# Performance work log

Hardware: AMD Instinct MI355X
Metric: run time of the kernel (lower is better)

Reference implementation:

```python
import jax, jax.numpy as jnp
import numpy as np

B, T, D, H = 4, 2048, 1024, 16
HD = D // H


def setup_inputs() -> dict:
    key = jax.random.key(0)
    kq, kk, kv, k1, k2, k3, k4 = jax.random.split(key, 7)
    q = jax.random.normal(kq, (B, T, D), dtype=jnp.float32)
    k = jax.random.normal(kk, (B, T, D), dtype=jnp.float32)
    v = jax.random.normal(kv, (B, T, D), dtype=jnp.float32)
    # causal mask, broadcast over heads: [B, 1, T, T]
    mask = jnp.broadcast_to(jnp.tril(jnp.ones((T, T), dtype=bool)), (B, 1, T, T))
    s = 0.02
    Wq = jax.random.normal(k1, (D, D), dtype=jnp.float32) * s
    Wk = jax.random.normal(k2, (D, D), dtype=jnp.float32) * s
    Wv = jax.random.normal(k3, (D, D), dtype=jnp.float32) * s
    Wo = jax.random.normal(k4, (D, D), dtype=jnp.float32) * s
    return {"q": q, "k": k, "v": v, "mask": mask,
            "Wq": Wq, "Wk": Wk, "Wv": Wv, "Wo": Wo}


def reference(q, k, v, mask, Wq, Wk, Wv, Wo):
    scale = HD ** -0.5
    # nn.Linear: y = x @ W.T  (bias=False)
    qh = (q @ Wq.T).reshape(B, T, H, HD).transpose(0, 2, 1, 3)  # [B,H,T,HD]
    kh = (k @ Wk.T).reshape(B, -1, H, HD).transpose(0, 2, 1, 3)
    vh = (v @ Wv.T).reshape(B, -1, H, HD).transpose(0, 2, 1, 3)
    scores = jnp.einsum('bhqd,bhkd->bhqk', qh, kh) * scale  # [B,H,T,T]
    # dropout p=0.0 -> identity (applied pre-mask in original)
    scores = jnp.where(mask, scores, -jnp.inf)
    probs = jax.nn.softmax(scores, axis=-1)
    attn = jnp.einsum('bhqk,bhkd->bhqd', probs, vh)  # [B,H,T,HD]
    attn = attn.transpose(0, 2, 1, 3).reshape(B, T, D)
    return attn @ Wo.T
```

## Files before the change

kernel.cpp:

```cpp
#include <hip/hip_runtime.h>
#include <stdint.h>

#define B_  4
#define T_  2048
#define D_  1024
#define H_  16
#define HD_ 64
#define KK_ 1024

typedef __bf16 bf16_t;
typedef __bf16 bf16x8 __attribute__((ext_vector_type(8)));
typedef float  f32x4  __attribute__((ext_vector_type(4)));
typedef float  f32x16 __attribute__((ext_vector_type(16)));

__device__ __forceinline__ uint16_t f2bf(float f) {
  uint32_t x = __float_as_uint(f);
  uint32_t r = (x + 0x7fffu + ((x >> 16) & 1u)) >> 16;
  return (uint16_t)r;
}

__device__ __forceinline__ uint32_t pack2(float a, float b) {
  return (uint32_t)f2bf(a) | ((uint32_t)f2bf(b) << 16);
}

__device__ __forceinline__ float exp2a(float x) {
  float r;
  asm("v_exp_f32 %0, %1" : "=v"(r) : "v"(x));
  return r;
}

__device__ __forceinline__ uint32_t cvtpk(float a, float b) {
  uint32_t r;
  asm("v_cvt_pk_bf16_f32 %0, %1, %2" : "=v"(r) : "v"(a), "v"(b));
  return r;
}

__device__ __forceinline__ void plswap(uint32_t& a, uint32_t& b) {
  asm("v_permlane32_swap_b32 %0, %1" : "+v"(a), "+v"(b));
}

__device__ __forceinline__ void gll16(const void* g, void* l) {
  __builtin_amdgcn_global_load_lds(
      (const __attribute__((address_space(1))) void*)g,
      (__attribute__((address_space(3))) void*)l, 16, 0, 0);
}

__global__ __launch_bounds__(256) void cvt3(const float* __restrict__ s0,
                                            const float* __restrict__ s1,
                                            const float* __restrict__ s2,
                                            uint16_t* __restrict__ d0,
                                            uint16_t* __restrict__ d1,
                                            uint16_t* __restrict__ d2) {
  const float* in = blockIdx.y == 0 ? s0 : (blockIdx.y == 1 ? s1 : s2);
  uint16_t* out = blockIdx.y == 0 ? d0 : (blockIdx.y == 1 ? d1 : d2);
  int i = (blockIdx.x * 256 + threadIdx.x) * 8;
  float4 a = *(const float4*)(in + i);
  float4 b = *(const float4*)(in + i + 4);
  uint4 u;
  u.x = pack2(a.x, a.y);
  u.y = pack2(a.z, a.w);
  u.z = pack2(b.x, b.y);
  u.w = pack2(b.z, b.w);
  *(uint4*)(out + i) = u;
}

__global__ __launch_bounds__(256) void cvtW(const float* __restrict__ s0,
                                            const float* __restrict__ s1,
                                            const float* __restrict__ s2,
                                            const float* __restrict__ s3,
                                            uint16_t* __restrict__ d0,
                                            uint16_t* __restrict__ d1,
                                            uint16_t* __restrict__ d2,
                                            uint16_t* __restrict__ d3) {
  const float* in = blockIdx.y == 0 ? s0 : (blockIdx.y == 1 ? s1 :
                    (blockIdx.y == 2 ? s2 : s3));
  uint16_t* out = blockIdx.y == 0 ? d0 : (blockIdx.y == 1 ? d1 :
                  (blockIdx.y == 2 ? d2 : d3));
  int i = (blockIdx.x * 256 + threadIdx.x) * 8;
  float4 a = *(const float4*)(in + i);
  float4 b = *(const float4*)(in + i + 4);
  uint4 u;
  u.x = pack2(a.x, a.y);
  u.y = pack2(a.z, a.w);
  u.z = pack2(b.x, b.y);
  u.w = pack2(b.z, b.w);
  *(uint4*)(out + i) = u;
}

__global__ __launch_bounds__(512, 2)
void gemm8(const uint16_t* __restrict__ a0, const uint16_t* __restrict__ a1,
           const uint16_t* __restrict__ a2, const uint16_t* __restrict__ w0,
           const uint16_t* __restrict__ w1, const uint16_t* __restrict__ w2,
           void* __restrict__ o0, void* __restrict__ o1, void* __restrict__ o2,
           int mode_base, float scale0) {
  __shared__ __align__(16) uint16_t Ab[3][128 * 64];
  __shared__ __align__(16) uint16_t Bb[3][256 * 64];

  const int nwg = gridDim.x;
  const int bid = blockIdx.x;
  const int cpx = nwg >> 3;
  const int swz = (bid & 7) * cpx + (bid >> 3);
  const int g = swz >> 8;
  const int r = swz & 255;
  const int mt = r >> 2, nt = r & 3;
  const int m0 = mt * 128, n0 = nt * 256;

  const uint16_t* A = g == 0 ? a0 : (g == 1 ? a1 : a2);
  const uint16_t* W = g == 0 ? w0 : (g == 1 ? w1 : w2);
  void* Out = g == 0 ? o0 : (g == 1 ? o1 : o2);
  const int mode = mode_base + g;
  const float scale = (mode == 0) ? scale0 : 1.0f;

  const int tid = threadIdx.x;
  const int wid = tid >> 6, lane = tid & 63;
  const int fr = lane & 15, fq = lane >> 4;
  const int wm = wid >> 2, wn = wid & 3;
  const int srow = lane >> 3, c8 = lane & 7;

  f32x4 acc[4][4];
#pragma unroll
  for (int i = 0; i < 4; ++i)
#pragma unroll
    for (int j = 0; j < 4; ++j) acc[i][j] = (f32x4){0.f, 0.f, 0.f, 0.f};

  const int NT = KK_ / 64;

#define STAGE(bi, t)                                                          \
  do {                                                                        \
    _Pragma("unroll")                                                         \
    for (int c = 0; c < 2; ++c) {                                             \
      int row = c * 64 + wid * 8 + srow;                                      \
      int sw = (c8 ^ (row & 7)) << 3;                                         \
      gll16(A + (size_t)(m0 + row) * KK_ + (t) * 64 + sw,                     \
            &Ab[bi][c * 4096 + wid * 512]);                                   \
    }                                                                         \
    _Pragma("unroll")                                                         \
    for (int c = 0; c < 4; ++c) {                                             \
      int row = c * 64 + wid * 8 + srow;                                      \
      int sw = (c8 ^ (row & 7)) << 3;                                         \
      gll16(W + (size_t)(n0 + row) * KK_ + (t) * 64 + sw,                     \
            &Bb[bi][c * 4096 + wid * 512]);                                   \
    }                                                                         \
  } while (0)

  STAGE(0, 0);
  STAGE(1, 1);
  asm volatile("s_waitcnt vmcnt(6)" ::: "memory");
  __builtin_amdgcn_s_barrier();

  int cur = 0;
  for (int t = 0; t < NT; ++t) {
    const uint16_t* Ac = &Ab[cur][0];
    const uint16_t* Bc = &Bb[cur][0];
    bf16x8 af0[4], bf0[4];
#pragma unroll
    for (int i = 0; i < 4; ++i) {
      int ra = wm * 64 + i * 16 + fr;
      af0[i] = *(const bf16x8*)&Ac[ra * 64 + ((fq ^ (ra & 7)) << 3)];
      int rb = wn * 64 + i * 16 + fr;
      bf0[i] = *(const bf16x8*)&Bc[rb * 64 + ((fq ^ (rb & 7)) << 3)];
    }
    if (t + 2 < NT) {
      int nb = cur + 2; if (nb >= 3) nb -= 3;
      STAGE(nb, t + 2);
    }
    bf16x8 af1[4], bf1[4];
#pragma unroll
    for (int i = 0; i < 4; ++i) {
      int ra = wm * 64 + i * 16 + fr;
      af1[i] = *(const bf16x8*)&Ac[ra * 64 + (((4 + fq) ^ (ra & 7)) << 3)];
      int rb = wn * 64 + i * 16 + fr;
      bf1[i] = *(const bf16x8*)&Bc[rb * 64 + (((4 + fq) ^ (rb & 7)) << 3)];
    }
    __builtin_amdgcn_s_setprio(1);
#pragma unroll
    for (int mf = 0; mf < 4; ++mf)
#pragma unroll
      for (int nf = 0; nf < 4; ++nf)
        acc[mf][nf] = __builtin_amdgcn_mfma_f32_16x16x32_bf16(af0[mf], bf0[nf],
                                                              acc[mf][nf], 0, 0, 0);
#pragma unroll
    for (int mf = 0; mf < 4; ++mf)
#pragma unroll
      for (int nf = 0; nf < 4; ++nf)
        acc[mf][nf] = __builtin_amdgcn_mfma_f32_16x16x32_bf16(af1[mf], bf1[nf],
                                                              acc[mf][nf], 0, 0, 0);
    __builtin_amdgcn_s_setprio(0);
    if (t + 1 < NT) {
      if (t + 2 < NT) {
        asm volatile("s_waitcnt vmcnt(6)" ::: "memory");
      } else {
        asm volatile("s_waitcnt vmcnt(0)" ::: "memory");
      }
      __builtin_amdgcn_s_barrier();
    }
    ++cur; if (cur == 3) cur = 0;
  }
#undef STAGE

#pragma unroll
  for (int mf = 0; mf < 4; ++mf) {
#pragma unroll
    for (int nf = 0; nf < 4; ++nf) {
      int m = m0 + wm * 64 + mf * 16 + fq * 4;
      int n = n0 + wn * 64 + nf * 16 + fr;
      if (mode == 2) {
        int b = m >> 11, t = m & (T_ - 1);
        int h = n >> 6, hd = n & 63;
        uint2 pk;
        pk.x = pack2(acc[mf][nf][0], acc[mf][nf][1]);
        pk.y = pack2(acc[mf][nf][2], acc[mf][nf][3]);
        uint16_t* dst = (uint16_t*)Out + ((((size_t)b * H_ + h) * HD_ + hd) * T_ + t);
        *(uint2*)dst = pk;
      } else if (mode == 3) {
#pragma unroll
        for (int rr = 0; rr < 4; ++rr)
          ((float*)Out)[(size_t)(m + rr) * D_ + n] = acc[mf][nf][rr];
      } else {
#pragma unroll
        for (int rr = 0; rr < 4; ++rr) {
          int mm = m + rr;
          int b = mm >> 11, t = mm & (T_ - 1);
          int h = n >> 6, hd = n & 63;
          ((uint16_t*)Out)[((((size_t)b * H_ + h) * T_ + t) << 6) + hd] =
              f2bf(acc[mf][nf][rr] * scale);
        }
      }
    }
  }
}

__global__ __launch_bounds__(512)
void attn_fwd(const uint16_t* __restrict__ Qh, const uint16_t* __restrict__ Kh,
              const uint16_t* __restrict__ Vt, uint16_t* __restrict__ O) {
  __shared__ __align__(16) uint16_t SB[6][64 * 64];

  const int tid = threadIdx.x, wid = tid >> 6, lane = tid & 63;
  const int ql = lane & 31, hi = lane >> 5;
  const int bid = blockIdx.x;
  const int qb = (T_ / 256 - 1) - (bid >> 6);
  const int bh = bid & 63;
  const int q0 = qb * 256;
  const int wq0 = q0 + wid * 32;
  const size_t hoff = (size_t)bh * T_ * HD_;
  const uint16_t* Qp = Qh + hoff;
  const uint16_t* Kp = Kh + hoff;
  const uint16_t* Vp = Vt + hoff;

  bf16x8 qf[4];
  {
    const uint16_t* qrow = Qp + (size_t)(wq0 + ql) * 64 + hi * 8;
#pragma unroll
    for (int ks = 0; ks < 4; ++ks) qf[ks] = *(const bf16x8*)(qrow + ks * 16);
  }

  float m = -1e30f, l = 0.f;
  f32x16 acc[2];
#pragma unroll
  for (int mo = 0; mo < 2; ++mo)
#pragma unroll
    for (int r = 0; r < 16; ++r) acc[mo][r] = 0.f;

  const int ntiles = 4 * qb + 4;

#define STAGE(buf, t)                                                        \
  do {                                                                       \
    int row = wid * 8 + (lane >> 3);                                         \
    int sw = ((lane & 7) ^ (row & 7)) << 3;                                  \
    gll16(Kp + (size_t)((t) * 64 + row) * 64 + sw, &SB[buf][wid * 512]);     \
    gll16(Vp + (size_t)row * T_ + (t) * 64 + sw, &SB[3 + (buf)][wid * 512]); \
  } while (0)

  STAGE(0, 0);
  if (ntiles > 1) STAGE(1, 1);
  asm volatile("s_waitcnt vmcnt(2)" ::: "memory");
  __builtin_amdgcn_s_barrier();

  int cur = 0;
  for (int it = 0; it < ntiles; ++it) {
    if (it + 2 < ntiles) {
      int nb = cur + 2; if (nb >= 3) nb -= 3;
      STAGE(nb, it + 2);
    }

    if (it * 64 <= wq0 + 31) {
      f32x16 st[2];
#pragma unroll
      for (int mm = 0; mm < 2; ++mm)
#pragma unroll
        for (int r = 0; r < 16; ++r) st[mm][r] = 0.f;
#pragma unroll
      for (int ks = 0; ks < 4; ++ks) {
#pragma unroll
        for (int mm = 0; mm < 2; ++mm) {
          int row = mm * 32 + ql;
          int ch = (ks * 2 + hi) ^ (row & 7);
          bf16x8 kf = *(const bf16x8*)&SB[cur][row * 64 + ch * 8];
          st[mm] = __builtin_amdgcn_mfma_f32_32x32x16_bf16(kf, qf[ks], st[mm], 0, 0, 0);
        }
      }

      if (it * 64 + 63 > wq0) {
        int qg = wq0 + ql;
#pragma unroll
        for (int mm = 0; mm < 2; ++mm)
#pragma unroll
          for (int r = 0; r < 16; ++r) {
            int kv = it * 64 + mm * 32 + (r & 3) + 8 * (r >> 2) + 4 * hi;
            if (kv > qg) st[mm][r] = -1e30f;
          }
      }

      float pm = st[0][0];
#pragma unroll
      for (int r = 1; r < 16; ++r) pm = fmaxf(pm, st[0][r]);
#pragma unroll
      for (int r = 0; r < 16; ++r) pm = fmaxf(pm, st[1][r]);
      pm = fmaxf(pm, __shfl_xor(pm, 32));

      if (__any(pm > m + 8.f)) {
        float mn = fmaxf(m, pm);
        float sf = exp2a(m - mn);
        m = mn;
        l *= sf;
#pragma unroll
        for (int mo = 0; mo < 2; ++mo)
#pragma unroll
          for (int r = 0; r < 16; ++r) acc[mo][r] *= sf;
      }

      float rs = 0.f;
#pragma unroll
      for (int mm = 0; mm < 2; ++mm)
#pragma unroll
        for (int r = 0; r < 16; ++r) {
          float p = exp2a(st[mm][r] - m);
          st[mm][r] = p;
          rs += p;
        }
      rs += __shfl_xor(rs, 32);
      l += rs;

      bf16x8 pf[4];
#pragma unroll
      for (int mm = 0; mm < 2; ++mm)
#pragma unroll
        for (int g = 0; g < 2; ++g) {
          uint32_t a1 = cvtpk(st[mm][8 * g + 0], st[mm][8 * g + 1]);
          uint32_t a2 = cvtpk(st[mm][8 * g + 2], st[mm][8 * g + 3]);
          uint32_t b1 = cvtpk(st[mm][8 * g + 4], st[mm][8 * g + 5]);
          uint32_t b2 = cvtpk(st[mm][8 * g + 6], st[mm][8 * g + 7]);
          plswap(a1, b1);
          plswap(a2, b2);
          union { uint32_t w[4]; bf16x8 v; } u;
          u.w[0] = a1; u.w[1] = a2; u.w[2] = b1; u.w[3] = b2;
          pf[mm * 2 + g] = u.v;
        }

#pragma unroll
      for (int ks = 0; ks < 4; ++ks) {
#pragma unroll
        for (int mo = 0; mo < 2; ++mo) {
          int row = mo * 32 + ql;
          int ch = (ks * 2 + hi) ^ (row & 7);
          bf16x8 vf = *(const bf16x8*)&SB[3 + cur][row * 64 + ch * 8];
          acc[mo] = __builtin_amdgcn_mfma_f32_32x32x16_bf16(vf, pf[ks], acc[mo], 0, 0, 0);
        }
      }
    }

    if (it + 1 < ntiles) {
      if (it + 2 < ntiles) {
        asm volatile("s_waitcnt vmcnt(2)" ::: "memory");
      } else {
        asm volatile("s_waitcnt vmcnt(0)" ::: "memory");
      }
      __builtin_amdgcn_s_barrier();
    }
    ++cur; if (cur == 3) cur = 0;
  }
#undef STAGE

  __syncthreads();
  uint16_t* ost = &SB[0][0];
  {
    float inv = 1.0f / l;
    uint16_t* wst = ost + wid * 2048;
#pragma unroll
    for (int mo = 0; mo < 2; ++mo)
#pragma unroll
      for (int r = 0; r < 16; r += 2) {
        int hd = mo * 32 + (r & 3) + 8 * (r >> 2) + 4 * hi;
        uint32_t pk = pack2(acc[mo][r] * inv, acc[mo][r + 1] * inv);
        int col = hd ^ ((ql & 7) << 3);
        *(uint32_t*)&wst[ql * 64 + col] = pk;
      }
  }
  __syncthreads();
  {
    int row = tid >> 1, half = tid & 1;
    int r7 = row & 7;
    int b = bh >> 4, h = bh & 15;
    size_t g = (size_t)(b * T_ + q0 + row) * D_ + h * 64 + half * 32;
#pragma unroll
    for (int j = 0; j < 4; ++j) {
      int cc = half * 4 + j;
      uint4 val = *(const uint4*)&ost[row * 64 + (cc ^ r7) * 8];
      *(uint4*)&O[g + j * 8] = val;
    }
  }
}

extern "C" void kernel_launch(void* const* d_in, const int* in_sizes, int n_in,
                              void* d_out, int out_size, void* d_ws, size_t ws_size,
                              hipStream_t stream) {
  (void)in_sizes; (void)n_in; (void)out_size; (void)ws_size;
  const float* q  = (const float*)d_in[0];
  const float* k  = (const float*)d_in[1];
  const float* v  = (const float*)d_in[2];
  const float* Wq = (const float*)d_in[4];
  const float* Wk = (const float*)d_in[5];
  const float* Wv = (const float*)d_in[6];
  const float* Wo = (const float*)d_in[7];

  uint8_t* ws = (uint8_t*)d_ws;
  const size_t MB = 1u << 20;
  uint16_t* WQB = (uint16_t*)(ws + 0 * MB);
  uint16_t* WKB = (uint16_t*)(ws + 2 * MB);
  uint16_t* WVB = (uint16_t*)(ws + 4 * MB);
  uint16_t* WOB = (uint16_t*)(ws + 6 * MB);
  uint16_t* XQ  = (uint16_t*)(ws + 8 * MB);
  uint16_t* XK  = (uint16_t*)(ws + 24 * MB);
  uint16_t* XV  = (uint16_t*)(ws + 40 * MB);
  uint16_t* QH  = (uint16_t*)(ws + 56 * MB);
  uint16_t* KH  = (uint16_t*)(ws + 72 * MB);
  uint16_t* VT  = (uint16_t*)(ws + 88 * MB);
  uint16_t* AC  = (uint16_t*)(ws + 8 * MB);

  cvt3<<<dim3(B_ * T_ * D_ / 2048, 3), 256, 0, stream>>>(q, k, v, XQ, XK, XV);
  cvtW<<<dim3(D_ * D_ / 2048, 4), 256, 0, stream>>>(Wq, Wk, Wv, Wo, WQB, WKB, WVB, WOB);

  const float qscale = 0.125f * 1.44269504088896340736f;

  gemm8<<<dim3(768), 512, 0, stream>>>(XQ, XK, XV, WQB, WKB, WVB,
                                       QH, KH, VT, 0, qscale);

  attn_fwd<<<dim3(T_ / 256 * 64), 512, 0, stream>>>(QH, KH, VT, AC);

  gemm8<<<dim3(256), 512, 0, stream>>>(AC, nullptr, nullptr, WOB, nullptr, nullptr,
                                       d_out, nullptr, nullptr, 3, 1.0f);
}
```

Before: 164.0 us.

## Fuse fp32-to-bf16 activation conversion into QKV projection GEMM loads

```diff
diff --git a/kernel.cpp b/kernel.cpp
--- a/kernel.cpp
+++ b/kernel.cpp
@@ -43,25 +43,6 @@
   __builtin_amdgcn_global_load_lds(
       (const __attribute__((address_space(1))) void*)g,
       (__attribute__((address_space(3))) void*)l, 16, 0, 0);
-}
-
-__global__ __launch_bounds__(256) void cvt3(const float* __restrict__ s0,
-                                            const float* __restrict__ s1,
-                                            const float* __restrict__ s2,
-                                            uint16_t* __restrict__ d0,
-                                            uint16_t* __restrict__ d1,
-                                            uint16_t* __restrict__ d2) {
-  const float* in = blockIdx.y == 0 ? s0 : (blockIdx.y == 1 ? s1 : s2);
-  uint16_t* out = blockIdx.y == 0 ? d0 : (blockIdx.y == 1 ? d1 : d2);
-  int i = (blockIdx.x * 256 + threadIdx.x) * 8;
-  float4 a = *(const float4*)(in + i);
-  float4 b = *(const float4*)(in + i + 4);
-  uint4 u;
-  u.x = pack2(a.x, a.y);
-  u.y = pack2(a.z, a.w);
-  u.z = pack2(b.x, b.y);
-  u.w = pack2(b.z, b.w);
-  *(uint4*)(out + i) = u;
 }
 
 __global__ __launch_bounds__(256) void cvtW(const float* __restrict__ s0,
@@ -87,9 +68,10 @@
   *(uint4*)(out + i) = u;
 }
 
+template <bool AF32>
 __global__ __launch_bounds__(512, 2)
-void gemm8(const uint16_t* __restrict__ a0, const uint16_t* __restrict__ a1,
-           const uint16_t* __restrict__ a2, const uint16_t* __restrict__ w0,
+void gemm8(const void* __restrict__ a0, const void* __restrict__ a1,
+           const void* __restrict__ a2, const uint16_t* __restrict__ w0,
            const uint16_t* __restrict__ w1, const uint16_t* __restrict__ w2,
            void* __restrict__ o0, void* __restrict__ o1, void* __restrict__ o2,
            int mode_base, float scale0) {
@@ -105,11 +87,13 @@
   const int mt = r >> 2, nt = r & 3;
   const int m0 = mt * 128, n0 = nt * 256;
 
-  const uint16_t* A = g == 0 ? a0 : (g == 1 ? a1 : a2);
+  const void* A = g == 0 ? a0 : (g == 1 ? a1 : a2);
   const uint16_t* W = g == 0 ? w0 : (g == 1 ? w1 : w2);
   void* Out = g == 0 ? o0 : (g == 1 ? o1 : o2);
   const int mode = mode_base + g;
   const float scale = (mode == 0) ? scale0 : 1.0f;
+  const float* A32 = (const float*)A;
+  const uint16_t* A16 = (const uint16_t*)A;
 
   const int tid = threadIdx.x;
   const int wid = tid >> 6, lane = tid & 63;
@@ -124,16 +108,47 @@
     for (int j = 0; j < 4; ++j) acc[i][j] = (f32x4){0.f, 0.f, 0.f, 0.f};
 
   const int NT = KK_ / 64;
-
-#define STAGE(bi, t)                                                          \
+  float4 ax[4];
+
+#define AISSUE(bi, t)                                                         \
   do {                                                                        \
-    _Pragma("unroll")                                                         \
-    for (int c = 0; c < 2; ++c) {                                             \
-      int row = c * 64 + wid * 8 + srow;                                      \
-      int sw = (c8 ^ (row & 7)) << 3;                                         \
-      gll16(A + (size_t)(m0 + row) * KK_ + (t) * 64 + sw,                     \
-            &Ab[bi][c * 4096 + wid * 512]);                                   \
+    if (AF32) {                                                               \
+      _Pragma("unroll")                                                       \
+      for (int c = 0; c < 2; ++c) {                                           \
+        int row = c * 64 + wid * 8 + srow;                                    \
+        int sw = (c8 ^ (row & 7)) << 3;                                       \
+        const float* src = A32 + (size_t)(m0 + row) * KK_ + (t) * 64 + sw;    \
+        ax[c * 2] = *(const float4*)src;                                      \
+        ax[c * 2 + 1] = *(const float4*)(src + 4);                            \
+      }                                                                       \
+    } else {                                                                  \
+      _Pragma("unroll")                                                       \
+      for (int c = 0; c < 2; ++c) {                                           \
+        int row = c * 64 + wid * 8 + srow;                                    \
+        int sw = (c8 ^ (row & 7)) << 3;                                       \
+        gll16(A16 + (size_t)(m0 + row) * KK_ + (t) * 64 + sw,                 \
+              &Ab[bi][c * 4096 + wid * 512]);                                 \
+      }                                                                       \
     }                                                                         \
+  } while (0)
+
+#define AWRITE(bi)                                                            \
+  do {                                                                        \
+    if (AF32) {                                                               \
+      _Pragma("unroll")                                                       \
+      for (int c = 0; c < 2; ++c) {                                           \
+        uint4 u;                                                              \
+        u.x = cvtpk(ax[c * 2].x, ax[c * 2].y);                                \
+        u.y = cvtpk(ax[c * 2].z, ax[c * 2].w);                                \
+        u.z = cvtpk(ax[c * 2 + 1].x, ax[c * 2 + 1].y);                        \
+        u.w = cvtpk(ax[c * 2 + 1].z, ax[c * 2 + 1].w);                        \
+        *(uint4*)&Ab[bi][c * 4096 + wid * 512 + lane * 8] = u;                \
+      }                                                                       \
+    }                                                                         \
+  } while (0)
+
+#define STAGEB(bi, t)                                                         \
+  do {                                                                        \
     _Pragma("unroll")                                                         \
     for (int c = 0; c < 4; ++c) {                                             \
       int row = c * 64 + wid * 8 + srow;                                      \
@@ -143,15 +158,32 @@
     }                                                                         \
   } while (0)
 
-  STAGE(0, 0);
-  STAGE(1, 1);
-  asm volatile("s_waitcnt vmcnt(6)" ::: "memory");
+  AISSUE(0, 0);
+  STAGEB(0, 0);
+  if (AF32) {
+    asm volatile("s_waitcnt vmcnt(4)" ::: "memory");
+    AWRITE(0);
+  }
+  AISSUE(1, 1);
+  STAGEB(1, 1);
+  if (AF32) {
+    asm volatile("s_waitcnt vmcnt(4)" ::: "memory");
+    AWRITE(1);
+  } else {
+    asm volatile("s_waitcnt vmcnt(6)" ::: "memory");
+  }
+  asm volatile("s_waitcnt lgkmcnt(0)" ::: "memory");
   __builtin_amdgcn_s_barrier();
 
   int cur = 0;
   for (int t = 0; t < NT; ++t) {
     const uint16_t* Ac = &Ab[cur][0];
     const uint16_t* Bc = &Bb[cur][0];
+    int nb = cur + 2; if (nb >= 3) nb -= 3;
+    if (t + 2 < NT) {
+      AISSUE(nb, t + 2);
+      STAGEB(nb, t + 2);
+    }
     bf16x8 af0[4], bf0[4];
 #pragma unroll
     for (int i = 0; i < 4; ++i) {
@@ -160,10 +192,6 @@
       int rb = wn * 64 + i * 16 + fr;
       bf0[i] = *(const bf16x8*)&Bc[rb * 64 + ((fq ^ (rb & 7)) << 3)];
     }
-    if (t + 2 < NT) {
-      int nb = cur + 2; if (nb >= 3) nb -= 3;
-      STAGE(nb, t + 2);
-    }
     bf16x8 af1[4], bf1[4];
 #pragma unroll
     for (int i = 0; i < 4; ++i) {
@@ -186,17 +214,25 @@
         acc[mf][nf] = __builtin_amdgcn_mfma_f32_16x16x32_bf16(af1[mf], bf1[nf],
                                                               acc[mf][nf], 0, 0, 0);
     __builtin_amdgcn_s_setprio(0);
+    if (t + 2 < NT) {
+      if (AF32) {
+        asm volatile("s_waitcnt vmcnt(4)" ::: "memory");
+        AWRITE(nb);
+      } else {
+        asm volatile("s_waitcnt vmcnt(6)" ::: "memory");
+      }
+    } else if (t + 1 < NT) {
+      asm volatile("s_waitcnt vmcnt(0)" ::: "memory");
+    }
     if (t + 1 < NT) {
-      if (t + 2 < NT) {
-        asm volatile("s_waitcnt vmcnt(6)" ::: "memory");
-      } else {
-        asm volatile("s_waitcnt vmcnt(0)" ::: "memory");
-      }
+      asm volatile("s_waitcnt lgkmcnt(0)" ::: "memory");
       __builtin_amdgcn_s_barrier();
     }
     ++cur; if (cur == 3) cur = 0;
   }
-#undef STAGE
+#undef AISSUE
+#undef AWRITE
+#undef STAGEB
 
 #pragma unroll
   for (int mf = 0; mf < 4; ++mf) {
@@ -429,24 +465,21 @@
   uint16_t* WKB = (uint16_t*)(ws + 2 * MB);
   uint16_t* WVB = (uint16_t*)(ws + 4 * MB);
   uint16_t* WOB = (uint16_t*)(ws + 6 * MB);
-  uint16_t* XQ  = (uint16_t*)(ws + 8 * MB);
-  uint16_t* XK  = (uint16_t*)(ws + 24 * MB);
-  uint16_t* XV  = (uint16_t*)(ws + 40 * MB);
   uint16_t* QH  = (uint16_t*)(ws + 56 * MB);
   uint16_t* KH  = (uint16_t*)(ws + 72 * MB);
   uint16_t* VT  = (uint16_t*)(ws + 88 * MB);
   uint16_t* AC  = (uint16_t*)(ws + 8 * MB);
 
-  cvt3<<<dim3(B_ * T_ * D_ / 2048, 3), 256, 0, stream>>>(q, k, v, XQ, XK, XV);
   cvtW<<<dim3(D_ * D_ / 2048, 4), 256, 0, stream>>>(Wq, Wk, Wv, Wo, WQB, WKB, WVB, WOB);
 
   const float qscale = 0.125f * 1.44269504088896340736f;
 
-  gemm8<<<dim3(768), 512, 0, stream>>>(XQ, XK, XV, WQB, WKB, WVB,
-                                       QH, KH, VT, 0, qscale);
+  gemm8<true><<<dim3(768), 512, 0, stream>>>(q, k, v, WQB, WKB, WVB,
+                                             QH, KH, VT, 0, qscale);
 
   attn_fwd<<<dim3(T_ / 256 * 64), 512, 0, stream>>>(QH, KH, VT, AC);
 
-  gemm8<<<dim3(256), 512, 0, stream>>>(AC, nullptr, nullptr, WOB, nullptr, nullptr,
-                                       d_out, nullptr, nullptr, 3, 1.0f);
-}
+  gemm8<false><<<dim3(256), 512, 0, stream>>>(AC, nullptr, nullptr,
+                                              WOB, nullptr, nullptr,
+                                              d_out, nullptr, nullptr, 3, 1.0f);
+}
```

After: 166.3 us. No clear change (+1.4%).

## Split GEMM staging around MFMA halves and pair KV tiles in attention

Applied to the files above, without the earlier changes.

```diff
diff --git a/kernel.cpp b/kernel.cpp
--- a/kernel.cpp
+++ b/kernel.cpp
@@ -125,7 +125,7 @@
 
   const int NT = KK_ / 64;
 
-#define STAGE(bi, t)                                                          \
+#define STAGEA(bi, t)                                                         \
   do {                                                                        \
     _Pragma("unroll")                                                         \
     for (int c = 0; c < 2; ++c) {                                             \
@@ -134,6 +134,10 @@
       gll16(A + (size_t)(m0 + row) * KK_ + (t) * 64 + sw,                     \
             &Ab[bi][c * 4096 + wid * 512]);                                   \
     }                                                                         \
+  } while (0)
+
+#define STAGEB(bi, t)                                                         \
+  do {                                                                        \
     _Pragma("unroll")                                                         \
     for (int c = 0; c < 4; ++c) {                                             \
       int row = c * 64 + wid * 8 + srow;                                      \
@@ -143,8 +147,10 @@
     }                                                                         \
   } while (0)
 
-  STAGE(0, 0);
-  STAGE(1, 1);
+  STAGEA(0, 0);
+  STAGEB(0, 0);
+  STAGEA(1, 1);
+  STAGEB(1, 1);
   asm volatile("s_waitcnt vmcnt(6)" ::: "memory");
   __builtin_amdgcn_s_barrier();
 
@@ -152,6 +158,8 @@
   for (int t = 0; t < NT; ++t) {
     const uint16_t* Ac = &Ab[cur][0];
     const uint16_t* Bc = &Bb[cur][0];
+    int nb = cur + 2; if (nb >= 3) nb -= 3;
+
     bf16x8 af0[4], bf0[4];
 #pragma unroll
     for (int i = 0; i < 4; ++i) {
@@ -160,10 +168,18 @@
       int rb = wn * 64 + i * 16 + fr;
       bf0[i] = *(const bf16x8*)&Bc[rb * 64 + ((fq ^ (rb & 7)) << 3)];
     }
-    if (t + 2 < NT) {
-      int nb = cur + 2; if (nb >= 3) nb -= 3;
-      STAGE(nb, t + 2);
-    }
+    if (t + 2 < NT) STAGEA(nb, t + 2);
+    __builtin_amdgcn_s_barrier();
+    __builtin_amdgcn_s_setprio(1);
+#pragma unroll
+    for (int mf = 0; mf < 4; ++mf)
+#pragma unroll
+      for (int nf = 0; nf < 4; ++nf)
+        acc[mf][nf] = __builtin_amdgcn_mfma_f32_16x16x32_bf16(af0[mf], bf0[nf],
+                                                              acc[mf][nf], 0, 0, 0);
+    __builtin_amdgcn_s_setprio(0);
+    __builtin_amdgcn_s_barrier();
+
     bf16x8 af1[4], bf1[4];
 #pragma unroll
     for (int i = 0; i < 4; ++i) {
@@ -172,13 +188,9 @@
       int rb = wn * 64 + i * 16 + fr;
       bf1[i] = *(const bf16x8*)&Bc[rb * 64 + (((4 + fq) ^ (rb & 7)) << 3)];
     }
+    if (t + 2 < NT) STAGEB(nb, t + 2);
+    __builtin_amdgcn_s_barrier();
     __builtin_amdgcn_s_setprio(1);
-#pragma unroll
-    for (int mf = 0; mf < 4; ++mf)
-#pragma unroll
-      for (int nf = 0; nf < 4; ++nf)
-        acc[mf][nf] = __builtin_amdgcn_mfma_f32_16x16x32_bf16(af0[mf], bf0[nf],
-                                                              acc[mf][nf], 0, 0, 0);
 #pragma unroll
     for (int mf = 0; mf < 4; ++mf)
 #pragma unroll
@@ -186,6 +198,7 @@
         acc[mf][nf] = __builtin_amdgcn_mfma_f32_16x16x32_bf16(af1[mf], bf1[nf],
                                                               acc[mf][nf], 0, 0, 0);
     __builtin_amdgcn_s_setprio(0);
+
     if (t + 1 < NT) {
       if (t + 2 < NT) {
         asm volatile("s_waitcnt vmcnt(6)" ::: "memory");
@@ -196,7 +209,8 @@
     }
     ++cur; if (cur == 3) cur = 0;
   }
-#undef STAGE
+#undef STAGEA
+#undef STAGEB
 
 #pragma unroll
   for (int mf = 0; mf < 4; ++mf) {
@@ -233,13 +247,15 @@
 __global__ __launch_bounds__(512)
 void attn_fwd(const uint16_t* __restrict__ Qh, const uint16_t* __restrict__ Kh,
               const uint16_t* __restrict__ Vt, uint16_t* __restrict__ O) {
-  __shared__ __align__(16) uint16_t SB[6][64 * 64];
+  __shared__ __align__(16) uint16_t SB[8][64 * 64];
 
   const int tid = threadIdx.x, wid = tid >> 6, lane = tid & 63;
   const int ql = lane & 31, hi = lane >> 5;
   const int bid = blockIdx.x;
-  const int qb = (T_ / 256 - 1) - (bid >> 6);
-  const int bh = bid & 63;
+  const int x = bid & 7;
+  const int e = bid >> 3;
+  const int qb = 7 - (e >> 3);
+  const int bh = ((e & 7) << 3) | x;
   const int q0 = qb * 256;
   const int wq0 = q0 + wid * 32;
   const size_t hoff = (size_t)bh * T_ * HD_;
@@ -261,123 +277,129 @@
 #pragma unroll
     for (int r = 0; r < 16; ++r) acc[mo][r] = 0.f;
 
-  const int ntiles = 4 * qb + 4;
+  const int npairs = 2 * qb + 2;
 
 #define STAGE(buf, t)                                                        \
   do {                                                                       \
     int row = wid * 8 + (lane >> 3);                                         \
     int sw = ((lane & 7) ^ (row & 7)) << 3;                                  \
     gll16(Kp + (size_t)((t) * 64 + row) * 64 + sw, &SB[buf][wid * 512]);     \
-    gll16(Vp + (size_t)row * T_ + (t) * 64 + sw, &SB[3 + (buf)][wid * 512]); \
+    gll16(Vp + (size_t)row * T_ + (t) * 64 + sw, &SB[4 + (buf)][wid * 512]); \
   } while (0)
 
   STAGE(0, 0);
-  if (ntiles > 1) STAGE(1, 1);
-  asm volatile("s_waitcnt vmcnt(2)" ::: "memory");
+  STAGE(1, 1);
+  asm volatile("s_waitcnt vmcnt(0)" ::: "memory");
   __builtin_amdgcn_s_barrier();
 
-  int cur = 0;
-  for (int it = 0; it < ntiles; ++it) {
-    if (it + 2 < ntiles) {
-      int nb = cur + 2; if (nb >= 3) nb -= 3;
-      STAGE(nb, it + 2);
-    }
-
-    if (it * 64 <= wq0 + 31) {
-      f32x16 st[2];
-#pragma unroll
-      for (int mm = 0; mm < 2; ++mm)
-#pragma unroll
-        for (int r = 0; r < 16; ++r) st[mm][r] = 0.f;
-#pragma unroll
-      for (int ks = 0; ks < 4; ++ks) {
-#pragma unroll
-        for (int mm = 0; mm < 2; ++mm) {
-          int row = mm * 32 + ql;
-          int ch = (ks * 2 + hi) ^ (row & 7);
-          bf16x8 kf = *(const bf16x8*)&SB[cur][row * 64 + ch * 8];
-          st[mm] = __builtin_amdgcn_mfma_f32_32x32x16_bf16(kf, qf[ks], st[mm], 0, 0, 0);
+  for (int j = 0; j < npairs; ++j) {
+    const int pb = (j & 1) * 2;
+    if (j + 1 < npairs) {
+      const int nb = ((j + 1) & 1) * 2;
+      STAGE(nb, 2 * j + 2);
+      STAGE(nb + 1, 2 * j + 3);
+    }
+
+#pragma unroll
+    for (int s = 0; s < 2; ++s) {
+      const int it = 2 * j + s;
+      if (it * 64 <= wq0 + 31) {
+        const uint16_t* Kl = &SB[pb + s][0];
+        const uint16_t* Vl = &SB[4 + pb + s][0];
+        f32x16 st[2];
+#pragma unroll
+        for (int mm = 0; mm < 2; ++mm)
+#pragma unroll
+          for (int r = 0; r < 16; ++r) st[mm][r] = 0.f;
+        __builtin_amdgcn_s_setprio(1);
+#pragma unroll
+        for (int ks = 0; ks < 4; ++ks) {
+#pragma unroll
+          for (int mm = 0; mm < 2; ++mm) {
+            int row = mm * 32 + ql;
+            int ch = (ks * 2 + hi) ^ (row & 7);
+            bf16x8 kf = *(const bf16x8*)&Kl[row * 64 + ch * 8];
+            st[mm] = __builtin_amdgcn_mfma_f32_32x32x16_bf16(kf, qf[ks], st[mm], 0, 0, 0);
+          }
         }
+        __builtin_amdgcn_s_setprio(0);
+
+        if (it * 64 + 63 > wq0) {
+          int qg = wq0 + ql;
+#pragma unroll
+          for (int mm = 0; mm < 2; ++mm)
+#pragma unroll
+            for (int r = 0; r < 16; ++r) {
+              int kv = it * 64 + mm * 32 + (r & 3) + 8 * (r >> 2) + 4 * hi;
+              if (kv > qg) st[mm][r] = -1e30f;
+            }
+        }
+
+        float pm = st[0][0];
+#pragma unroll
+        for (int r = 1; r < 16; ++r) pm = fmaxf(pm, st[0][r]);
+#pragma unroll
+        for (int r = 0; r < 16; ++r) pm = fmaxf(pm, st[1][r]);
+        pm = fmaxf(pm, __shfl_xor(pm, 32));
+
+        if (__any(pm > m + 8.f)) {
+          float mn = fmaxf(m, pm);
+          float sf = exp2a(m - mn);
+          m = mn;
+          l *= sf;
+#pragma unroll
+          for (int mo = 0; mo < 2; ++mo)
+#pragma unroll
+            for (int r = 0; r < 16; ++r) acc[mo][r] *= sf;
+        }
+
+        float rs = 0.f;
+#pragma unroll
+        for (int mm = 0; mm < 2; ++mm)
+#pragma unroll
+          for (int r = 0; r < 16; ++r) {
+            float p = exp2a(st[mm][r] - m);
+            st[mm][r] = p;
+            rs += p;
+          }
+        rs += __shfl_xor(rs, 32);
+        l += rs;
+
+        bf16x8 pf[4];
+#pragma unroll
+        for (int mm = 0; mm < 2; ++mm)
+#pragma unroll
+          for (int g = 0; g < 2; ++g) {
+            uint32_t a1 = cvtpk(st[mm][8 * g + 0], st[mm][8 * g + 1]);
+            uint32_t a2 = cvtpk(st[mm][8 * g + 2], st[mm][8 * g + 3]);
+            uint32_t b1 = cvtpk(st[mm][8 * g + 4], st[mm][8 * g + 5]);
+            uint32_t b2 = cvtpk(st[mm][8 * g + 6], st[mm][8 * g + 7]);
+            plswap(a1, b1);
+            plswap(a2, b2);
+            union { uint32_t w[4]; bf16x8 v; } u;
+            u.w[0] = a1; u.w[1] = a2; u.w[2] = b1; u.w[3] = b2;
+            pf[mm * 2 + g] = u.v;
+          }
+
+        __builtin_amdgcn_s_setprio(1);
+#pragma unroll
+        for (int ks = 0; ks < 4; ++ks) {
+#pragma unroll
+          for (int mo = 0; mo < 2; ++mo) {
+            int row = mo * 32 + ql;
+            int ch = (ks * 2 + hi) ^ (row & 7);
+            bf16x8 vf = *(const bf16x8*)&Vl[row * 64 + ch * 8];
+            acc[mo] = __builtin_amdgcn_mfma_f32_32x32x16_bf16(vf, pf[ks], acc[mo], 0, 0, 0);
+          }
+        }
+        __builtin_amdgcn_s_setprio(0);
       }
-
-      if (it * 64 + 63 > wq0) {
-        int qg = wq0 + ql;
-#pragma unroll
-        for (int mm = 0; mm < 2; ++mm)
-#pragma unroll
-          for (int r = 0; r < 16; ++r) {
-            int kv = it * 64 + mm * 32 + (r & 3) + 8 * (r >> 2) + 4 * hi;
-            if (kv > qg) st[mm][r] = -1e30f;
-          }
-      }
-
-      float pm = st[0][0];
-#pragma unroll
-      for (int r = 1; r < 16; ++r) pm = fmaxf(pm, st[0][r]);
-#pragma unroll
-      for (int r = 0; r < 16; ++r) pm = fmaxf(pm, st[1][r]);
-      pm = fmaxf(pm, __shfl_xor(pm, 32));
-
-      if (__any(pm > m + 8.f)) {
-        float mn = fmaxf(m, pm);
-        float sf = exp2a(m - mn);
-        m = mn;
-        l *= sf;
-#pragma unroll
-        for (int mo = 0; mo < 2; ++mo)
-#pragma unroll
-          for (int r = 0; r < 16; ++r) acc[mo][r] *= sf;
-      }
-
-      float rs = 0.f;
-#pragma unroll
-      for (int mm = 0; mm < 2; ++mm)
-#pragma unroll
-        for (int r = 0; r < 16; ++r) {
-          float p = exp2a(st[mm][r] - m);
-          st[mm][r] = p;
-          rs += p;
-        }
-      rs += __shfl_xor(rs, 32);
-      l += rs;
-
-      bf16x8 pf[4];
-#pragma unroll
-      for (int mm = 0; mm < 2; ++mm)
-#pragma unroll
-        for (int g = 0; g < 2; ++g) {
-          uint32_t a1 = cvtpk(st[mm][8 * g + 0], st[mm][8 * g + 1]);
-          uint32_t a2 = cvtpk(st[mm][8 * g + 2], st[mm][8 * g + 3]);
-          uint32_t b1 = cvtpk(st[mm][8 * g + 4], st[mm][8 * g + 5]);
-          uint32_t b2 = cvtpk(st[mm][8 * g + 6], st[mm][8 * g + 7]);
-          plswap(a1, b1);
-          plswap(a2, b2);
-          union { uint32_t w[4]; bf16x8 v; } u;
-          u.w[0] = a1; u.w[1] = a2; u.w[2] = b1; u.w[3] = b2;
-          pf[mm * 2 + g] = u.v;
-        }
-
-#pragma unroll
-      for (int ks = 0; ks < 4; ++ks) {
-#pragma unroll
-        for (int mo = 0; mo < 2; ++mo) {
-          int row = mo * 32 + ql;
-          int ch = (ks * 2 + hi) ^ (row & 7);
-          bf16x8 vf = *(const bf16x8*)&SB[3 + cur][row * 64 + ch * 8];
-          acc[mo] = __builtin_amdgcn_mfma_f32_32x32x16_bf16(vf, pf[ks], acc[mo], 0, 0, 0);
-        }
-      }
-    }
-
-    if (it + 1 < ntiles) {
-      if (it + 2 < ntiles) {
-        asm volatile("s_waitcnt vmcnt(2)" ::: "memory");
-      } else {
-        asm volatile("s_waitcnt vmcnt(0)" ::: "memory");
-      }
+    }
+
+    if (j + 1 < npairs) {
+      asm volatile("s_waitcnt vmcnt(0)" ::: "memory");
       __builtin_amdgcn_s_barrier();
     }
-    ++cur; if (cur == 3) cur = 0;
   }
 #undef STAGE
 
@@ -403,10 +425,10 @@
     int b = bh >> 4, h = bh & 15;
     size_t g = (size_t)(b * T_ + q0 + row) * D_ + h * 64 + half * 32;
 #pragma unroll
-    for (int j = 0; j < 4; ++j) {
-      int cc = half * 4 + j;
+    for (int j2 = 0; j2 < 4; ++j2) {
+      int cc = half * 4 + j2;
       uint4 val = *(const uint4*)&ost[row * 64 + (cc ^ r7) * 8];
-      *(uint4*)&O[g + j * 8] = val;
+      *(uint4*)&O[g + j2 * 8] = val;
     }
   }
 }
@@ -437,7 +459,8 @@
   uint16_t* VT  = (uint16_t*)(ws + 88 * MB);
   uint16_t* AC  = (uint16_t*)(ws + 8 * MB);
 
-  cvt3<<<dim3(B_ * T_ * D_ / 2048, 3), 256, 0, stream>>>(q, k, v, XQ, XK, XV);
+  const int nBig = B_ * T_ * D_;
+  cvt3<<<dim3(nBig / 2048, 3), 256, 0, stream>>>(q, k, v, XQ, XK, XV);
   cvtW<<<dim3(D_ * D_ / 2048, 4), 256, 0, stream>>>(Wq, Wk, Wv, Wo, WQB, WKB, WVB, WOB);
 
   const float qscale = 0.125f * 1.44269504088896340736f;
@@ -445,7 +468,7 @@
   gemm8<<<dim3(768), 512, 0, stream>>>(XQ, XK, XV, WQB, WKB, WVB,
                                        QH, KH, VT, 0, qscale);
 
-  attn_fwd<<<dim3(T_ / 256 * 64), 512, 0, stream>>>(QH, KH, VT, AC);
+  attn_fwd<<<dim3(512), 512, 0, stream>>>(QH, KH, VT, AC);
 
   gemm8<<<dim3(256), 512, 0, stream>>>(AC, nullptr, nullptr, WOB, nullptr, nullptr,
                                        d_out, nullptr, nullptr, 3, 1.0f);
```

Result: slower. 174.3 us (+6.3%).

## Load GEMM weight fragments directly to registers, stage only A in LDS

Applied to the files above, without the earlier changes.

```diff
diff --git a/kernel.cpp b/kernel.cpp
--- a/kernel.cpp
+++ b/kernel.cpp
@@ -87,23 +87,22 @@
   *(uint4*)(out + i) = u;
 }
 
-__global__ __launch_bounds__(512, 2)
-void gemm8(const uint16_t* __restrict__ a0, const uint16_t* __restrict__ a1,
-           const uint16_t* __restrict__ a2, const uint16_t* __restrict__ w0,
-           const uint16_t* __restrict__ w1, const uint16_t* __restrict__ w2,
-           void* __restrict__ o0, void* __restrict__ o1, void* __restrict__ o2,
-           int mode_base, float scale0) {
-  __shared__ __align__(16) uint16_t Ab[3][128 * 64];
-  __shared__ __align__(16) uint16_t Bb[3][256 * 64];
+__global__ __launch_bounds__(256, 2)
+void gemmBR(const uint16_t* __restrict__ a0, const uint16_t* __restrict__ a1,
+            const uint16_t* __restrict__ a2, const uint16_t* __restrict__ w0,
+            const uint16_t* __restrict__ w1, const uint16_t* __restrict__ w2,
+            void* __restrict__ o0, void* __restrict__ o1, void* __restrict__ o2,
+            int mode_base, float scale0) {
+  __shared__ __align__(16) uint16_t Ab[2][128 * 64];
 
   const int nwg = gridDim.x;
   const int bid = blockIdx.x;
   const int cpx = nwg >> 3;
   const int swz = (bid & 7) * cpx + (bid >> 3);
-  const int g = swz >> 8;
-  const int r = swz & 255;
-  const int mt = r >> 2, nt = r & 3;
-  const int m0 = mt * 128, n0 = nt * 256;
+  const int g = swz >> 9;
+  const int r = swz & 511;
+  const int mt = r >> 3, nt = r & 7;
+  const int m0 = mt * 128, n0 = nt * 128;
 
   const uint16_t* A = g == 0 ? a0 : (g == 1 ? a1 : a2);
   const uint16_t* W = g == 0 ? w0 : (g == 1 ? w1 : w2);
@@ -114,7 +113,7 @@
   const int tid = threadIdx.x;
   const int wid = tid >> 6, lane = tid & 63;
   const int fr = lane & 15, fq = lane >> 4;
-  const int wm = wid >> 2, wn = wid & 3;
+  const int wm = wid >> 1, wn = wid & 1;
   const int srow = lane >> 3, c8 = lane & 7;
 
   f32x4 acc[4][4];
@@ -124,79 +123,78 @@
     for (int j = 0; j < 4; ++j) acc[i][j] = (f32x4){0.f, 0.f, 0.f, 0.f};
 
   const int NT = KK_ / 64;
-
-#define STAGE(bi, t)                                                          \
+  bf16x8 bfA[4][2], bfB[4][2];
+
+#define STAGEA(s, t)                                                          \
   do {                                                                        \
     _Pragma("unroll")                                                         \
-    for (int c = 0; c < 2; ++c) {                                             \
-      int row = c * 64 + wid * 8 + srow;                                      \
+    for (int c = 0; c < 4; ++c) {                                             \
+      int row = wid * 32 + c * 8 + srow;                                      \
       int sw = (c8 ^ (row & 7)) << 3;                                         \
       gll16(A + (size_t)(m0 + row) * KK_ + (t) * 64 + sw,                     \
-            &Ab[bi][c * 4096 + wid * 512]);                                   \
-    }                                                                         \
-    _Pragma("unroll")                                                         \
-    for (int c = 0; c < 4; ++c) {                                             \
-      int row = c * 64 + wid * 8 + srow;                                      \
-      int sw = (c8 ^ (row & 7)) << 3;                                         \
-      gll16(W + (size_t)(n0 + row) * KK_ + (t) * 64 + sw,                     \
-            &Bb[bi][c * 4096 + wid * 512]);                                   \
+            &Ab[s][(wid * 32 + c * 8) * 64]);                                 \
     }                                                                         \
   } while (0)
 
-  STAGE(0, 0);
-  STAGE(1, 1);
-  asm volatile("s_waitcnt vmcnt(6)" ::: "memory");
+#define BLOAD(bf, t)                                                          \
+  do {                                                                        \
+    _Pragma("unroll")                                                         \
+    for (int nf = 0; nf < 4; ++nf)                                            \
+      _Pragma("unroll")                                                       \
+      for (int ks = 0; ks < 2; ++ks)                                          \
+        bf[nf][ks] = *(const bf16x8*)(W +                                     \
+            (size_t)(n0 + wn * 64 + nf * 16 + fr) * KK_ + (t) * 64 +          \
+            (ks * 4 + fq) * 8);                                               \
+  } while (0)
+
+  STAGEA(0, 0);
+  __builtin_amdgcn_sched_barrier(0);
+  BLOAD(bfA, 0);
+  __builtin_amdgcn_sched_barrier(0);
+  asm volatile("s_waitcnt vmcnt(8)" ::: "memory");
   __builtin_amdgcn_s_barrier();
 
-  int cur = 0;
-  for (int t = 0; t < NT; ++t) {
-    const uint16_t* Ac = &Ab[cur][0];
-    const uint16_t* Bc = &Bb[cur][0];
-    bf16x8 af0[4], bf0[4];
-#pragma unroll
-    for (int i = 0; i < 4; ++i) {
-      int ra = wm * 64 + i * 16 + fr;
-      af0[i] = *(const bf16x8*)&Ac[ra * 64 + ((fq ^ (ra & 7)) << 3)];
-      int rb = wn * 64 + i * 16 + fr;
-      bf0[i] = *(const bf16x8*)&Bc[rb * 64 + ((fq ^ (rb & 7)) << 3)];
-    }
-    if (t + 2 < NT) {
-      int nb = cur + 2; if (nb >= 3) nb -= 3;
-      STAGE(nb, t + 2);
-    }
-    bf16x8 af1[4], bf1[4];
-#pragma unroll
-    for (int i = 0; i < 4; ++i) {
-      int ra = wm * 64 + i * 16 + fr;
-      af1[i] = *(const bf16x8*)&Ac[ra * 64 + (((4 + fq) ^ (ra & 7)) << 3)];
-      int rb = wn * 64 + i * 16 + fr;
-      bf1[i] = *(const bf16x8*)&Bc[rb * 64 + (((4 + fq) ^ (rb & 7)) << 3)];
-    }
-    __builtin_amdgcn_s_setprio(1);
-#pragma unroll
-    for (int mf = 0; mf < 4; ++mf)
-#pragma unroll
-      for (int nf = 0; nf < 4; ++nf)
-        acc[mf][nf] = __builtin_amdgcn_mfma_f32_16x16x32_bf16(af0[mf], bf0[nf],
-                                                              acc[mf][nf], 0, 0, 0);
-#pragma unroll
-    for (int mf = 0; mf < 4; ++mf)
-#pragma unroll
-      for (int nf = 0; nf < 4; ++nf)
-        acc[mf][nf] = __builtin_amdgcn_mfma_f32_16x16x32_bf16(af1[mf], bf1[nf],
-                                                              acc[mf][nf], 0, 0, 0);
-    __builtin_amdgcn_s_setprio(0);
-    if (t + 1 < NT) {
-      if (t + 2 < NT) {
-        asm volatile("s_waitcnt vmcnt(6)" ::: "memory");
-      } else {
-        asm volatile("s_waitcnt vmcnt(0)" ::: "memory");
-      }
-      __builtin_amdgcn_s_barrier();
-    }
-    ++cur; if (cur == 3) cur = 0;
-  }
-#undef STAGE
+#define BODY(t, bfU, bfL)                                                     \
+  do {                                                                        \
+    if ((t) + 1 < NT) {                                                       \
+      STAGEA(((t) + 1) & 1, (t) + 1);                                         \
+      __builtin_amdgcn_sched_barrier(0);                                      \
+      BLOAD(bfL, (t) + 1);                                                    \
+      __builtin_amdgcn_sched_barrier(0);                                      \
+    }                                                                         \
+    const uint16_t* Ac = &Ab[(t) & 1][0];                                     \
+    bf16x8 af[4][2];                                                          \
+    _Pragma("unroll")                                                         \
+    for (int mf = 0; mf < 4; ++mf) {                                          \
+      int ra = wm * 64 + mf * 16 + fr;                                        \
+      _Pragma("unroll")                                                       \
+      for (int ks = 0; ks < 2; ++ks)                                          \
+        af[mf][ks] =                                                          \
+            *(const bf16x8*)&Ac[ra * 64 + (((ks * 4 + fq) ^ (ra & 7)) << 3)]; \
+    }                                                                         \
+    __builtin_amdgcn_s_setprio(1);                                            \
+    _Pragma("unroll")                                                         \
+    for (int ks = 0; ks < 2; ++ks)                                            \
+      _Pragma("unroll")                                                       \
+      for (int mf = 0; mf < 4; ++mf)                                          \
+        _Pragma("unroll")                                                     \
+        for (int nf = 0; nf < 4; ++nf)                                        \
+          acc[mf][nf] = __builtin_amdgcn_mfma_f32_16x16x32_bf16(              \
+              af[mf][ks], bfU[nf][ks], acc[mf][nf], 0, 0, 0);                 \
+    __builtin_amdgcn_s_setprio(0);                                            \
+    if ((t) + 1 < NT) {                                                       \
+      asm volatile("s_waitcnt vmcnt(8)" ::: "memory");     \
+      __builtin_amdgcn_s_barrier();                                           \
+    }                                                                         \
+  } while (0)
+
+  for (int tt = 0; tt < NT; tt += 2) {
+    BODY(tt, bfA, bfB);
+    BODY(tt + 1, bfB, bfA);
+  }
+#undef BODY
+#undef BLOAD
+#undef STAGEA
 
 #pragma unroll
   for (int mf = 0; mf < 4; ++mf) {
@@ -403,10 +401,10 @@
     int b = bh >> 4, h = bh & 15;
     size_t g = (size_t)(b * T_ + q0 + row) * D_ + h * 64 + half * 32;
 #pragma unroll
-    for (int j = 0; j < 4; ++j) {
-      int cc = half * 4 + j;
+    for (int j2 = 0; j2 < 4; ++j2) {
+      int cc = half * 4 + j2;
       uint4 val = *(const uint4*)&ost[row * 64 + (cc ^ r7) * 8];
-      *(uint4*)&O[g + j * 8] = val;
+      *(uint4*)&O[g + j2 * 8] = val;
     }
   }
 }
@@ -437,16 +435,18 @@
   uint16_t* VT  = (uint16_t*)(ws + 88 * MB);
   uint16_t* AC  = (uint16_t*)(ws + 8 * MB);
 
-  cvt3<<<dim3(B_ * T_ * D_ / 2048, 3), 256, 0, stream>>>(q, k, v, XQ, XK, XV);
+  const int nBig = B_ * T_ * D_;
+  cvt3<<<dim3(nBig / 2048, 3), 256, 0, stream>>>(q, k, v, XQ, XK, XV);
   cvtW<<<dim3(D_ * D_ / 2048, 4), 256, 0, stream>>>(Wq, Wk, Wv, Wo, WQB, WKB, WVB, WOB);
 
   const float qscale = 0.125f * 1.44269504088896340736f;
 
-  gemm8<<<dim3(768), 512, 0, stream>>>(XQ, XK, XV, WQB, WKB, WVB,
-                                       QH, KH, VT, 0, qscale);
+  gemmBR<<<dim3(1536), 256, 0, stream>>>(XQ, XK, XV, WQB, WKB, WVB,
+                                         QH, KH, VT, 0, qscale);
 
   attn_fwd<<<dim3(T_ / 256 * 64), 512, 0, stream>>>(QH, KH, VT, AC);
 
-  gemm8<<<dim3(256), 512, 0, stream>>>(AC, nullptr, nullptr, WOB, nullptr, nullptr,
-                                       d_out, nullptr, nullptr, 3, 1.0f);
-}
+  gemmBR<<<dim3(512), 256, 0, stream>>>(AC, nullptr, nullptr,
+                                        WOB, nullptr, nullptr,
+                                        d_out, nullptr, nullptr, 3, 1.0f);
+}
```

After: 232.2 us. 41.6% more time.
